# Optimization experiments

Hardware: AMD Instinct MI355X
Metric: run time of the kernel (lower is better)

The kernel has to match this reference:

```python
import jax, jax.numpy as jnp
import numpy as np

RATIO = 0.25
K = 32
LN_EPS = 1e-5


def _fps(xyz, npoint):
    """Farthest point sampling. xyz [B,N,3] -> idx [B,npoint] (int32).
    Deterministic start at index 0 (torch version uses randint)."""
    B, N, _ = xyz.shape
    init_dist = jnp.full((B, N), 1e10, dtype=xyz.dtype)
    init_far = jnp.zeros((B,), dtype=jnp.int32)

    def step(carry, _):
        dist, far = carry
        centroid = jnp.take_along_axis(xyz, far[:, None, None], axis=1)  # [B,1,3]
        d = jnp.sum((xyz - centroid) ** 2, axis=-1)                      # [B,N]
        dist = jnp.minimum(dist, d)
        new_far = jnp.argmax(dist, axis=-1).astype(jnp.int32)
        return (dist, new_far), far  # emit the index BEFORE update (matches torch)

    _, idx = jax.lax.scan(step, (init_dist, init_far), None, length=npoint)
    return idx.T  # [B,npoint]


def _knn(x, k):
    """k-nearest neighbors by squared distance. x [B,S,3] -> idx [B,S,k]."""
    xx = jnp.sum(x ** 2, axis=-1, keepdims=True)            # [B,S,1]
    inner = jnp.einsum('bsd,btd->bst', x, x)                # [B,S,S]
    neg_sqdist = 2.0 * inner - xx - jnp.swapaxes(xx, 1, 2)  # -||xi-xj||^2
    return jax.lax.top_k(neg_sqdist, k)[1]                  # [B,S,k]


def _gather(pts, idx):
    """pts [B,N,C], idx [B,...] -> [B,...,C]."""
    B = pts.shape[0]
    flat = idx.reshape(B, -1)
    out = jnp.take_along_axis(pts, flat[..., None], axis=1)
    return out.reshape(idx.shape + (pts.shape[-1],))


def _forward(xyz, features, W1, b1, gamma, beta, W2, b2):
    B, N, _ = xyz.shape
    npoint = max(int(N * RATIO), 1)
    k = min(K, N)

    fps_idx = _fps(xyz, npoint)                 # [B,S]
    new_xyz = _gather(xyz, fps_idx)             # [B,S,3]

    # NOTE: module computes knn(xyz) + gathers but never uses them (dead code) -> skipped.
    # Faithful quirk: knn over new_xyz gives indices in [0,npoint) which the
    # original then uses to index the ORIGINAL xyz/features.
    fps_nb_idx = _knn(new_xyz, min(K, N))       # [B,S,k]
    nb_xyz = _gather(xyz, fps_nb_idx)           # [B,S,k,3]
    nb_feat = _gather(features, fps_nb_idx)     # [B,S,k,C]

    pos_diff = nb_xyz - new_xyz[:, :, None, :]
    combined = jnp.concatenate([nb_feat, pos_diff], axis=-1)  # [B,S,k,C+3]

    h = combined @ W1 + b1                      # [B,S,k,O]
    mu = jnp.mean(h, axis=-1, keepdims=True)
    var = jnp.var(h, axis=-1, keepdims=True)
    h = (h - mu) * jax.lax.rsqrt(var + LN_EPS) * gamma + beta
    h = jax.nn.relu(h)
    h = h @ W2 + b2
    new_features = jnp.max(h, axis=2)           # [B,S,O]
    return new_xyz, new_features


def setup_inputs() -> dict:
    key = jax.random.key(0)
    ks = jax.random.split(key, 4)
    B, N, C, O = 4, 16384, 64, 128
    xyz = jax.random.normal(ks[0], (B, N, 3), dtype=jnp.float32)
    features = jax.random.normal(ks[1], (B, N, C), dtype=jnp.float32)
    W1 = jax.random.normal(ks[2], (C + 3, O), dtype=jnp.float32) * 0.05
    b1 = jnp.zeros((O,), jnp.float32)
    gamma = jnp.ones((O,), jnp.float32)
    beta = jnp.zeros((O,), jnp.float32)
    W2 = jax.random.normal(ks[3], (O, O), dtype=jnp.float32) * 0.05
    b2 = jnp.zeros((O,), jnp.float32)
    return {"xyz": xyz, "features": features, "W1": W1, "b1": b1,
            "gamma": gamma, "beta": beta, "W2": W2, "b2": b2}


def reference(xyz, features, W1, b1, gamma, beta, W2, b2):
    return _forward(xyz, features, W1, b1, gamma, beta, W2, b2)
```

## Files before the change

kernel.cpp:

```cpp
#include <hip/hip_runtime.h>
#include <cstdint>

#define B_ 4
#define N_ 16384
#define C_ 64
#define O_ 128
#define S_ 4096
#define K_ 32
#define CK_ 67

__launch_bounds__(512, 2)
__global__ void fps_kernel(const float* __restrict__ xyz,
                           float* __restrict__ new_xyz) {
#pragma clang fp contract(off)
  const int b = blockIdx.x;
  const int t = threadIdx.x;
  const float* base = xyz + (size_t)b * N_ * 3;
  constexpr int PPT = N_ / 512;
  float px[PPT], py[PPT], pz[PPT], dist[PPT];
#pragma unroll
  for (int j = 0; j < PPT; ++j) {
    int p = j * 512 + t;
    px[j] = base[p * 3 + 0];
    py[j] = base[p * 3 + 1];
    pz[j] = base[p * 3 + 2];
    dist[j] = 1e10f;
  }
  __shared__ unsigned long long s_part[2][8];
  const int lane = t & 63;
  const int wid = t >> 6;
  float fx = base[0], fy = base[1], fz = base[2];
  for (int s = 0; s < S_; ++s) {
    if (t == 0) {
      float* o = new_xyz + ((size_t)b * S_ + s) * 3;
      o[0] = fx; o[1] = fy; o[2] = fz;
    }
    float bv = -1.0f;
    int bi = 0;
#pragma unroll
    for (int j = 0; j < PPT; ++j) {
      float dx = px[j] - fx;
      float dy = py[j] - fy;
      float dz = pz[j] - fz;
      float d = dx * dx + dy * dy + dz * dz;
      float m = fminf(dist[j], d);
      dist[j] = m;
      if (m > bv) { bv = m; bi = j * 512 + t; }
    }
    unsigned long long key =
        ((unsigned long long)__float_as_uint(bv) << 32) | (unsigned)(~bi);
#pragma unroll
    for (int off = 1; off <= 32; off <<= 1) {
      unsigned long long ok = __shfl_xor(key, off);
      if (ok > key) key = ok;
    }
    const int buf = s & 1;
    if (lane == 0) s_part[buf][wid] = key;
    __syncthreads();
    unsigned long long kb = s_part[buf][0];
#pragma unroll
    for (int w = 1; w < 8; ++w) {
      unsigned long long ok = s_part[buf][w];
      if (ok > kb) kb = ok;
    }
    const int pw = (int)(~(unsigned)kb);
    fx = base[pw * 3 + 0];
    fy = base[pw * 3 + 1];
    fz = base[pw * 3 + 2];
  }
}

__launch_bounds__(256, 2)
__global__ void knn_kernel(const float* __restrict__ new_xyz,
                           int* __restrict__ knn_idx) {
  const int b = blockIdx.y;
  const int t = threadIdx.x;
  const int q = blockIdx.x * 256 + t;
  __shared__ float sx[S_], sy[S_], sz[S_], sn[S_];
  const float* nb = new_xyz + (size_t)b * S_ * 3;
  for (int i = t; i < S_; i += 256) {
    float x = nb[i * 3 + 0], y = nb[i * 3 + 1], z = nb[i * 3 + 2];
    sx[i] = x; sy[i] = y; sz[i] = z;
    sn[i] = fmaf(z, z, fmaf(y, y, x * x));
  }
  __syncthreads();
  const float qx = sx[q], qy = sy[q], qz = sz[q], qn = sn[q];
  unsigned long long kv[K_];
#pragma unroll
  for (int j = 0; j < K_; ++j) kv[j] = 0ull;
  for (int i = 0; i < S_; ++i) {
    float inner = fmaf(sz[i], qz, fmaf(sy[i], qy, sx[i] * qx));
    float score = (2.0f * inner - qn) - sn[i];
    unsigned u = __float_as_uint(score);
    u ^= (unsigned)((int)u >> 31) | 0x80000000u;
    unsigned long long nk = ((unsigned long long)u << 32) | (unsigned)(~i);
    if (nk > kv[K_ - 1]) {
#pragma unroll
      for (int j = K_ - 1; j >= 1; --j) {
        bool upPrev = nk > kv[j - 1];
        kv[j] = upPrev ? kv[j - 1] : ((nk > kv[j]) ? nk : kv[j]);
      }
      if (nk > kv[0]) kv[0] = nk;
    }
  }
#pragma unroll
  for (int j = 0; j < K_; ++j)
    knn_idx[((size_t)b * S_ + q) * K_ + j] = (int)(~(unsigned)kv[j]);
}

#define W1S 76
#define W2S 132
#define CLS 72
#define HPS 132

__launch_bounds__(256, 1)
__global__ void mlp_kernel(const float* __restrict__ xyz,
                           const float* __restrict__ features,
                           const float* __restrict__ new_xyz,
                           const int* __restrict__ knn_idx,
                           const float* __restrict__ W1,
                           const float* __restrict__ b1,
                           const float* __restrict__ gamma,
                           const float* __restrict__ beta,
                           const float* __restrict__ W2,
                           const float* __restrict__ b2,
                           float* __restrict__ out_feat) {
  __shared__ float w1T[O_][W1S];
  __shared__ float w2T[O_][W2S];
  __shared__ float c_l[K_][CLS];
  __shared__ float hp[K_][HPS];
  __shared__ float pmaxl[8][O_];

  const int t = threadIdx.x;
  const int g = t >> 5;
  const int cg = t & 31;

  for (int e = t; e < CK_ * O_; e += 256) {
    int k = e >> 7, c = e & (O_ - 1);
    w1T[c][k] = W1[e];
  }
  if (t < O_) {
#pragma unroll
    for (int k = CK_; k < 68; ++k) w1T[t][k] = 0.0f;
  }
  for (int e = t; e < O_ * O_; e += 256) {
    int k = e >> 7, c = e & (O_ - 1);
    w2T[c][k] = W2[e];
  }
  float bb1[4], gm[4], bt[4], bb2 = 0.0f;
#pragma unroll
  for (int j = 0; j < 4; ++j) {
    bb1[j] = b1[cg + 32 * j];
    gm[j] = gamma[cg + 32 * j];
    bt[j] = beta[cg + 32 * j];
  }
  if (t < O_) bb2 = b2[t];

  const int bs0 = blockIdx.x * 64;
  const int b = bs0 >> 12;
  const float* fb = features + (size_t)b * N_ * C_;
  const float* xb = xyz + (size_t)b * N_ * 3;

  __syncthreads();

  for (int is = 0; is < 64; ++is) {
    const int bs = bs0 + is;
    const float qx = new_xyz[(size_t)bs * 3 + 0];
    const float qy = new_xyz[(size_t)bs * 3 + 1];
    const float qz = new_xyz[(size_t)bs * 3 + 2];

    for (int e = t; e < K_ * 68; e += 256) {
      int r = e >> 6;
      r = e / 68;
      int k = e - r * 68;
      int nbi = knn_idx[(size_t)bs * K_ + r];
      float v;
      if (k < C_) {
        v = fb[(size_t)nbi * C_ + k];
      } else if (k < CK_) {
        float coord = xb[nbi * 3 + (k - C_)];
        float qq = (k == C_) ? qx : ((k == C_ + 1) ? qy : qz);
        v = coord - qq;
      } else {
        v = 0.0f;
      }
      c_l[r][k] = v;
    }
    __syncthreads();

    float h[4][4];
#pragma unroll
    for (int i = 0; i < 4; ++i)
#pragma unroll
      for (int j = 0; j < 4; ++j) h[i][j] = 0.0f;
#pragma unroll
    for (int kc = 0; kc < 17; ++kc) {
      float4 w[4], a[4];
#pragma unroll
      for (int j = 0; j < 4; ++j)
        w[j] = *reinterpret_cast<const float4*>(&w1T[cg + 32 * j][kc * 4]);
#pragma unroll
      for (int i = 0; i < 4; ++i)
        a[i] = *reinterpret_cast<const float4*>(&c_l[4 * g + i][kc * 4]);
#pragma unroll
      for (int i = 0; i < 4; ++i)
#pragma unroll
        for (int j = 0; j < 4; ++j) {
          h[i][j] = fmaf(a[i].x, w[j].x, h[i][j]);
          h[i][j] = fmaf(a[i].y, w[j].y, h[i][j]);
          h[i][j] = fmaf(a[i].z, w[j].z, h[i][j]);
          h[i][j] = fmaf(a[i].w, w[j].w, h[i][j]);
        }
    }
#pragma unroll
    for (int i = 0; i < 4; ++i)
#pragma unroll
      for (int j = 0; j < 4; ++j) h[i][j] += bb1[j];

#pragma unroll
    for (int i = 0; i < 4; ++i) {
      float s1 = (h[i][0] + h[i][1]) + (h[i][2] + h[i][3]);
      float s2 = ((h[i][0] * h[i][0] + h[i][1] * h[i][1]) +
                  (h[i][2] * h[i][2] + h[i][3] * h[i][3]));
#pragma unroll
      for (int off = 1; off <= 16; off <<= 1) {
        s1 += __shfl_xor(s1, off);
        s2 += __shfl_xor(s2, off);
      }
      float mu = s1 * (1.0f / 128.0f);
      float va = fmaf(mu, -mu, s2 * (1.0f / 128.0f));
      float rs = rsqrtf(va + 1e-5f);
#pragma unroll
      for (int j = 0; j < 4; ++j) {
        float hv = fmaf((h[i][j] - mu) * rs, gm[j], bt[j]);
        hp[4 * g + i][cg + 32 * j] = fmaxf(hv, 0.0f);
      }
    }
    __syncthreads();

    float acc[4][4];
#pragma unroll
    for (int i = 0; i < 4; ++i)
#pragma unroll
      for (int j = 0; j < 4; ++j) acc[i][j] = 0.0f;
#pragma unroll 8
    for (int kc = 0; kc < 32; ++kc) {
      float4 w[4], a[4];
#pragma unroll
      for (int j = 0; j < 4; ++j)
        w[j] = *reinterpret_cast<const float4*>(&w2T[cg + 32 * j][kc * 4]);
#pragma unroll
      for (int i = 0; i < 4; ++i)
        a[i] = *reinterpret_cast<const float4*>(&hp[4 * g + i][kc * 4]);
#pragma unroll
      for (int i = 0; i < 4; ++i)
#pragma unroll
        for (int j = 0; j < 4; ++j) {
          acc[i][j] = fmaf(a[i].x, w[j].x, acc[i][j]);
          acc[i][j] = fmaf(a[i].y, w[j].y, acc[i][j]);
          acc[i][j] = fmaf(a[i].z, w[j].z, acc[i][j]);
          acc[i][j] = fmaf(a[i].w, w[j].w, acc[i][j]);
        }
    }
#pragma unroll
    for (int j = 0; j < 4; ++j) {
      float pm = fmaxf(fmaxf(acc[0][j], acc[1][j]), fmaxf(acc[2][j], acc[3][j]));
      pmaxl[g][cg + 32 * j] = pm;
    }
    __syncthreads();

    if (t < O_) {
      float m = pmaxl[0][t];
#pragma unroll
      for (int w = 1; w < 8; ++w) m = fmaxf(m, pmaxl[w][t]);
      out_feat[(size_t)bs * O_ + t] = m + bb2;
    }
    __syncthreads();
  }
}

extern "C" void kernel_launch(void* const* d_in, const int* in_sizes, int n_in,
                              void* d_out, int out_size, void* d_ws, size_t ws_size,
                              hipStream_t stream) {
  const float* xyz      = (const float*)d_in[0];
  const float* features = (const float*)d_in[1];
  const float* W1       = (const float*)d_in[2];
  const float* b1       = (const float*)d_in[3];
  const float* gamma    = (const float*)d_in[4];
  const float* beta     = (const float*)d_in[5];
  const float* W2       = (const float*)d_in[6];
  const float* b2       = (const float*)d_in[7];

  float* out      = (float*)d_out;
  float* new_xyz  = out;
  float* new_feat = out + (size_t)B_ * S_ * 3;
  int* knn_idx = (int*)d_ws;

  fps_kernel<<<B_, 512, 0, stream>>>(xyz, new_xyz);
  knn_kernel<<<dim3(S_ / 256, B_), 256, 0, stream>>>(new_xyz, knn_idx);
  mlp_kernel<<<B_ * S_ / 64, 256, 0, stream>>>(xyz, features, new_xyz, knn_idx,
                                               W1, b1, gamma, beta, W2, b2,
                                               new_feat);
}
```

Measured before the change: 9.785 ms.

## Spatially sort points by Morton cell and prune FPS updates with bounding boxes

Adds a counting-sort kernel that orders each batch's points by a 16^3 Morton grid cell, so each FPS thread owns a spatially compact chunk of 32 points with a per-thread bounding box. On each FPS step a thread skips its distance update when the box's lower-bound distance to the new centroid cannot lower its current maximum, reusing its cached best key. The winning coordinates now pass through shared memory instead of being reloaded from global memory. Tie-breaking uses original indices packed into 14 bits, and the fixed grid range assumes roughly normal inputs. The skip test carries a small floating-point safety margin.

```diff
diff --git a/kernel.cpp b/kernel.cpp
--- a/kernel.cpp
+++ b/kernel.cpp
@@ -1,5 +1,7 @@
 #include <hip/hip_runtime.h>
 #include <cstdint>
+
+typedef unsigned long long ull;
 
 #define B_ 4
 #define N_ 16384
@@ -9,64 +11,155 @@
 #define K_ 32
 #define CK_ 67
 
+__device__ __forceinline__ unsigned part3_4(unsigned v) {
+  return (v & 1u) | ((v & 2u) << 2) | ((v & 4u) << 4) | ((v & 8u) << 6);
+}
+
+__launch_bounds__(1024, 1)
+__global__ void sort_kernel(const float* __restrict__ xyz,
+                            float4* __restrict__ sorted) {
+  const int b = blockIdx.x, t = threadIdx.x;
+  const int lane = t & 63, wid = t >> 6;
+  __shared__ unsigned hist[4096];
+  __shared__ unsigned wsum[16];
+  for (int i = t; i < 4096; i += 1024) hist[i] = 0u;
+  __syncthreads();
+  const float* base = xyz + (size_t)b * N_ * 3;
+  int cell[16];
+#pragma unroll
+  for (int j = 0; j < 16; ++j) {
+    int p = j * 1024 + t;
+    float x = base[p * 3 + 0], y = base[p * 3 + 1], z = base[p * 3 + 2];
+    int cx = (int)floorf((x + 6.0f) * (16.0f / 12.0f));
+    int cy = (int)floorf((y + 6.0f) * (16.0f / 12.0f));
+    int cz = (int)floorf((z + 6.0f) * (16.0f / 12.0f));
+    cx = min(max(cx, 0), 15); cy = min(max(cy, 0), 15); cz = min(max(cz, 0), 15);
+    int m = (int)(part3_4((unsigned)cx) | (part3_4((unsigned)cy) << 1) |
+                  (part3_4((unsigned)cz) << 2));
+    cell[j] = m;
+    atomicAdd(&hist[m], 1u);
+  }
+  __syncthreads();
+  unsigned h0 = hist[4 * t + 0], h1 = hist[4 * t + 1];
+  unsigned h2 = hist[4 * t + 2], h3 = hist[4 * t + 3];
+  unsigned s4 = h0 + h1 + h2 + h3;
+  unsigned inc = s4;
+#pragma unroll
+  for (int off = 1; off < 64; off <<= 1) {
+    unsigned n = __shfl_up(inc, off);
+    if (lane >= off) inc += n;
+  }
+  if (lane == 63) wsum[wid] = inc;
+  __syncthreads();
+  if (t < 16) {
+    unsigned v = wsum[t], iv = v;
+#pragma unroll
+    for (int off = 1; off < 16; off <<= 1) {
+      unsigned n = __shfl_up(iv, off);
+      if (t >= off) iv += n;
+    }
+    wsum[t] = iv - v;
+  }
+  __syncthreads();
+  unsigned st = wsum[wid] + (inc - s4);
+  hist[4 * t + 0] = st;
+  hist[4 * t + 1] = st + h0;
+  hist[4 * t + 2] = st + h0 + h1;
+  hist[4 * t + 3] = st + h0 + h1 + h2;
+  __syncthreads();
+#pragma unroll
+  for (int j = 0; j < 16; ++j) {
+    int p = j * 1024 + t;
+    float x = base[p * 3 + 0], y = base[p * 3 + 1], z = base[p * 3 + 2];
+    unsigned pos = atomicAdd(&hist[cell[j]], 1u);
+    float4 o;
+    o.x = x; o.y = y; o.z = z; o.w = __uint_as_float((unsigned)p);
+    sorted[(size_t)b * N_ + pos] = o;
+  }
+}
+
 __launch_bounds__(512, 2)
 __global__ void fps_kernel(const float* __restrict__ xyz,
+                           const float4* __restrict__ sorted,
                            float* __restrict__ new_xyz) {
 #pragma clang fp contract(off)
-  const int b = blockIdx.x;
-  const int t = threadIdx.x;
-  const float* base = xyz + (size_t)b * N_ * 3;
-  constexpr int PPT = N_ / 512;
-  float px[PPT], py[PPT], pz[PPT], dist[PPT];
-#pragma unroll
-  for (int j = 0; j < PPT; ++j) {
-    int p = j * 512 + t;
-    px[j] = base[p * 3 + 0];
-    py[j] = base[p * 3 + 1];
-    pz[j] = base[p * 3 + 2];
+  const int b = blockIdx.x, t = threadIdx.x;
+  const int lane = t & 63, wid = t >> 6;
+  const float4* sb = sorted + (size_t)b * N_;
+  float px[32], py[32], pz[32], dist[32];
+  unsigned po2[16];
+#pragma unroll
+  for (int j = 0; j < 32; ++j) {
+    float4 v = sb[32 * t + j];
+    px[j] = v.x; py[j] = v.y; pz[j] = v.z;
     dist[j] = 1e10f;
-  }
-  __shared__ unsigned long long s_part[2][8];
-  const int lane = t & 63;
-  const int wid = t >> 6;
-  float fx = base[0], fy = base[1], fz = base[2];
+    unsigned o = __float_as_uint(v.w);
+    if ((j & 1) == 0) po2[j >> 1] = o; else po2[j >> 1] |= (o << 16);
+  }
+  float lox = px[0], hix = px[0], loy = py[0], hiy = py[0], loz = pz[0], hiz = pz[0];
+#pragma unroll
+  for (int j = 1; j < 32; ++j) {
+    lox = fminf(lox, px[j]); hix = fmaxf(hix, px[j]);
+    loy = fminf(loy, py[j]); hiy = fmaxf(hiy, py[j]);
+    loz = fminf(loz, pz[j]); hiz = fmaxf(hiz, pz[j]);
+  }
+  __shared__ ull s_key[2][8];
+  __shared__ float s_cd[2][8][3];
+  const float* ob = xyz + (size_t)b * N_ * 3;
+  float fx = ob[0], fy = ob[1], fz = ob[2];
+  ull mykey = ((ull)__float_as_uint(1e10f)) << 28;
+  float mybx = 0.f, myby = 0.f, mybz = 0.f;
   for (int s = 0; s < S_; ++s) {
     if (t == 0) {
       float* o = new_xyz + ((size_t)b * S_ + s) * 3;
       o[0] = fx; o[1] = fy; o[2] = fz;
     }
-    float bv = -1.0f;
-    int bi = 0;
-#pragma unroll
-    for (int j = 0; j < PPT; ++j) {
-      float dx = px[j] - fx;
-      float dy = py[j] - fy;
-      float dz = pz[j] - fz;
-      float d = dx * dx + dy * dy + dz * dz;
-      float m = fminf(dist[j], d);
-      dist[j] = m;
-      if (m > bv) { bv = m; bi = j * 512 + t; }
-    }
-    unsigned long long key =
-        ((unsigned long long)__float_as_uint(bv) << 32) | (unsigned)(~bi);
-#pragma unroll
-    for (int off = 1; off <= 32; off <<= 1) {
-      unsigned long long ok = __shfl_xor(key, off);
-      if (ok > key) key = ok;
+    float dxm = fmaxf(fmaxf(lox - fx, fx - hix), 0.0f);
+    float dym = fmaxf(fmaxf(loy - fy, fy - hiy), 0.0f);
+    float dzm = fmaxf(fmaxf(loz - fz, fz - hiz), 0.0f);
+    float lb = dxm * dxm + dym * dym + dzm * dzm;
+    float bmax = __uint_as_float((unsigned)(mykey >> 28));
+    if (!(lb * 0.99998f >= bmax)) {
+      float bv = -1.0f;
+      unsigned bo = 0xFFFFFFFFu;
+      int bp = 0;
+      float bx = px[0], by = py[0], bz = pz[0];
+#pragma unroll
+      for (int j = 0; j < 32; ++j) {
+        float dx = px[j] - fx;
+        float dy = py[j] - fy;
+        float dz = pz[j] - fz;
+        float d = dx * dx + dy * dy + dz * dz;
+        float m = fminf(dist[j], d);
+        dist[j] = m;
+        unsigned og = (po2[j >> 1] >> (16 * (j & 1))) & 0xFFFFu;
+        bool better = (m > bv) || ((m == bv) && (og < bo));
+        if (better) { bv = m; bo = og; bp = j; bx = px[j]; by = py[j]; bz = pz[j]; }
+      }
+      mykey = (((ull)__float_as_uint(bv)) << 28) |
+              (((ull)((~bo) & 0x3FFFu)) << 14) | (unsigned)(32 * t + bp);
+      mybx = bx; myby = by; mybz = bz;
+    }
+    ull k = mykey;
+#pragma unroll
+    for (int off = 1; off < 64; off <<= 1) {
+      ull o = __shfl_xor(k, off);
+      if (o > k) k = o;
     }
     const int buf = s & 1;
-    if (lane == 0) s_part[buf][wid] = key;
-    __syncthreads();
-    unsigned long long kb = s_part[buf][0];
+    if (k == mykey) {
+      s_key[buf][wid] = k;
+      s_cd[buf][wid][0] = mybx; s_cd[buf][wid][1] = myby; s_cd[buf][wid][2] = mybz;
+    }
+    __syncthreads();
+    ull kb = s_key[buf][0];
+    int bw = 0;
 #pragma unroll
     for (int w = 1; w < 8; ++w) {
-      unsigned long long ok = s_part[buf][w];
-      if (ok > kb) kb = ok;
-    }
-    const int pw = (int)(~(unsigned)kb);
-    fx = base[pw * 3 + 0];
-    fy = base[pw * 3 + 1];
-    fz = base[pw * 3 + 2];
+      ull o = s_key[buf][w];
+      if (o > kb) { kb = o; bw = w; }
+    }
+    fx = s_cd[buf][bw][0]; fy = s_cd[buf][bw][1]; fz = s_cd[buf][bw][2];
   }
 }
 
@@ -170,8 +263,7 @@
     const float qz = new_xyz[(size_t)bs * 3 + 2];
 
     for (int e = t; e < K_ * 68; e += 256) {
-      int r = e >> 6;
-      r = e / 68;
+      int r = e / 68;
       int k = e - r * 68;
       int nbi = knn_idx[(size_t)bs * K_ + r];
       float v;
@@ -295,8 +387,10 @@
   float* new_xyz  = out;
   float* new_feat = out + (size_t)B_ * S_ * 3;
   int* knn_idx = (int*)d_ws;
-
-  fps_kernel<<<B_, 512, 0, stream>>>(xyz, new_xyz);
+  float4* sorted = (float4*)((char*)d_ws + (size_t)B_ * S_ * K_ * 4);
+
+  sort_kernel<<<B_, 1024, 0, stream>>>(xyz, sorted);
+  fps_kernel<<<B_, 512, 0, stream>>>(xyz, sorted, new_xyz);
   knn_kernel<<<dim3(S_ / 256, B_), 256, 0, stream>>>(new_xyz, knn_idx);
   mlp_kernel<<<B_ * S_ / 64, 256, 0, stream>>>(xyz, features, new_xyz, knn_idx,
                                                W1, b1, gamma, beta, W2, b2,
```

Measured after the change: 18.37 ms. 1.88x slower.
